# Performance work log

Measured on AMD Instinct MI355X. Metric: run time of the kernel, lower is better.

The kernel has to match this reference:

```python
import jax, jax.numpy as jnp
from jax import lax
import numpy as np

D_IN = 12      # latent_dim / flow input_dim
HALF = 6       # coupling split
HID = 192      # flow_hidden_dim
LAYERS = 24    # flow_layers
N_BASES = 66
SYM = 12       # symmetry_dim
OUT_DIM = 6    # rows of tangent frame J_p
B = 16384
EPS_P = 1e-3
CLAMP = 2.0    # soft clamp for 'exp_clamp' scale map: s = CLAMP*tanh(raw/CLAMP)


def _mlp(z1, p):
    W1, b1, W2, b2, W3, b3 = p
    h = jax.nn.relu(z1 @ W1.T + b1)
    h = jax.nn.relu(h @ W2.T + b2)
    return h @ W3.T + b3


def _coupling_fwd(z, p):
    # AffineCouplingBlock (split->affine->merge) followed by Permute(swap)
    z1, z2 = z[..., :HALF], z[..., HALF:]
    prm = _mlp(z1, p)
    shift, sraw = prm[..., 0::2], prm[..., 1::2]
    s = CLAMP * jnp.tanh(sraw / CLAMP)
    z2 = z2 * jnp.exp(s) + shift
    # merge [z1, z2'] then swap halves -> [z2', z1]
    return jnp.concatenate([z2, z1], axis=-1), jnp.sum(s, axis=-1)


def _coupling_inv(z, p):
    # inverse of Permute(swap) is swap again
    z = jnp.concatenate([z[..., HALF:], z[..., :HALF]], axis=-1)
    z1, z2 = z[..., :HALF], z[..., HALF:]
    prm = _mlp(z1, p)
    shift, sraw = prm[..., 0::2], prm[..., 1::2]
    s = CLAMP * jnp.tanh(sraw / CLAMP)
    z2 = (z2 - shift) * jnp.exp(-s)
    return jnp.concatenate([z1, z2], axis=-1), -jnp.sum(s, axis=-1)


def flow_forward(z, params):
    def step(c, p):
        z, ld = c
        z, d = _coupling_fwd(z, p)
        return (z, ld + d), None
    (z, ld), _ = lax.scan(step, (z, jnp.zeros(z.shape[:-1], z.dtype)), params)
    return z, ld


def flow_inverse(y, params):
    def step(c, p):
        z, ld = c
        z, d = _coupling_inv(z, p)
        return (z, ld + d), None
    (z, ld), _ = lax.scan(step, (y, jnp.zeros(y.shape[:-1], y.dtype)), params, reverse=True)
    return z, ld


def pullback_tangent(z, v, params):
    # J[b] = v[b] @ d(flow_forward)/dz at z[b], via per-sample vjp
    def one(zb, vb):
        _, vjp_fn = jax.vjp(lambda zz: flow_forward(zz, params)[0], zb)
        return jax.vmap(lambda r: vjp_fn(r)[0])(vb)
    return jax.vmap(one)(z, v)


def kl_divergence(J_p, J_q, log_var_diag):
    b, out_dim, in_dim = J_p.shape
    J_p = J_p / jnp.sqrt(jnp.sum(J_p * J_p))  # global normalization
    S_p = jnp.einsum('bni,bmi->bnm', J_p, J_p)
    S_q = jnp.einsum('bin,bim->bnm', J_q, J_q)
    S_pq = jnp.einsum('bni,bmi->bnm', J_p[:, :, :SYM], J_q)
    D = jnp.exp(-log_var_diag)  # (in_dim,)
    I_p = jnp.eye(out_dim, dtype=J_p.dtype)
    I_q = jnp.eye(SYM, dtype=J_q.dtype)
    M = S_p + EPS_P * I_p
    H = S_q + D[:SYM] * I_q
    norm_M = jnp.maximum(jnp.mean(jnp.diagonal(M, axis1=-2, axis2=-1), -1), 1e-6)
    norm_H = jnp.maximum(jnp.mean(jnp.diagonal(H, axis1=-2, axis2=-1), -1), 1e-6)
    M = M + 1e-3 * norm_M[:, None, None] * I_p
    H = H + 1e-3 * norm_H[:, None, None] * I_q
    Db = D + 1e-3 * norm_H[:, None]  # (b, in_dim)
    trace_p = jnp.einsum('bij,bij,bj->b', J_p, J_p, Db)
    trace_q = jnp.einsum('bij,bij->b', J_q, J_q)
    trace_pq = jnp.einsum('bij,bij->b', S_pq, S_pq)
    trace = (EPS_P + 1e-3 * norm_M) * (jnp.sum(Db, -1) + trace_q) + trace_p + trace_pq
    L_M = jnp.linalg.cholesky(M)
    L_H = jnp.linalg.cholesky(H)
    logdet_M = 2.0 * jnp.sum(jnp.log(jnp.diagonal(L_M, axis1=-2, axis2=-1)), -1)
    logdet_H = 2.0 * jnp.sum(jnp.log(jnp.diagonal(L_H, axis1=-2, axis2=-1)), -1)
    logdet_p = logdet_M + (in_dim - out_dim) * np.float32(np.log(EPS_P))
    logdet_q = logdet_H + jnp.sum(jnp.log(Db[:, SYM:]), -1)
    logdet = -(logdet_p + logdet_q)
    return 0.5 * (trace + logdet - in_dim)


def setup_inputs() -> dict:
    key = jax.random.key(0)
    ks = jax.random.split(key, 10)
    y = jax.random.normal(ks[0], (B, D_IN), jnp.float32)
    J_p = jax.random.normal(ks[1], (B, OUT_DIM, D_IN), jnp.float32)
    sc = 0.05
    W1 = sc * jax.random.normal(ks[2], (LAYERS, HID, HALF), jnp.float32)
    b1 = sc * jax.random.normal(ks[3], (LAYERS, HID), jnp.float32)
    W2 = sc * jax.random.normal(ks[4], (LAYERS, HID, HID), jnp.float32)
    b2 = sc * jax.random.normal(ks[5], (LAYERS, HID), jnp.float32)
    W3 = sc * jax.random.normal(ks[6], (LAYERS, D_IN, HID), jnp.float32)
    b3 = sc * jax.random.normal(ks[7], (LAYERS, D_IN), jnp.float32)
    Wsym = (1.0 / np.sqrt(SYM)) * jax.random.normal(ks[8], (N_BASES, SYM, SYM), jnp.float32)
    log_var_diag = jnp.zeros((D_IN,), jnp.float32)
    return {"y": y, "J_p": J_p, "W1": W1, "b1": b1, "W2": W2, "b2": b2,
            "W3": W3, "b3": b3, "Wsym": Wsym, "log_var_diag": log_var_diag}


def reference(y, J_p, W1, b1, W2, b2, W3, b3, Wsym, log_var_diag):
    params = (W1, b1, W2, b2, W3, b3)
    z, ld = flow_inverse(y, params)
    # DiagGaussian(trainable=False) base log prob = standard normal
    log_prob = ld - 0.5 * D_IN * np.float32(np.log(2.0 * np.pi)) - 0.5 * jnp.sum(z * z, -1)
    Jp = pullback_tangent(z, J_p, params)
    A = Wsym - jnp.swapaxes(Wsym, -1, -2)
    J_q = jnp.einsum('bi,mji->bmj', z[:, :SYM], A)
    kl = kl_divergence(Jp, J_q, log_var_diag)
    return (log_prob, kl)
```

## Files before the change

kernel.cpp:

```cpp
#include <hip/hip_runtime.h>
#include <hip/hip_bf16.h>
#include <math.h>

#define BTOT   16384
#define NLAYER 24
#define HID    192
#define NDIN   12
#define NBASE  66
#define EPSP   1e-3f
#define EPB    32

#define EST 200
#define W3ST 17
#define OB_H1  0
#define OB_G   12800
#define OB_R   89600
#define OB_W1  98816
#define OB_W3F 101888
#define OB_PRM 114944
#define OB_GZ  118016
#define OB_Z1  122624
#define OB_LD  123392
#define OB_ZQ  123520
#define OB_RED 123648
#define SMEM_BYTES 123680

typedef __attribute__((ext_vector_type(8))) short s8v;
typedef __attribute__((ext_vector_type(4))) float f4v;
#define MFMA16(a,b,c) __builtin_amdgcn_mfma_f32_16x16x32_bf16(a,b,c,0,0,0)

__device__ __forceinline__ unsigned short f2bf(float f) {
  unsigned u = __builtin_bit_cast(unsigned, f);
  u += 0x7fffu + ((u >> 16) & 1u);
  return (unsigned short)(u >> 16);
}
__device__ __forceinline__ float bf2f(unsigned short h) {
  unsigned u = ((unsigned)h) << 16;
  return __builtin_bit_cast(float, u);
}
__device__ __forceinline__ unsigned pk2(float a, float b) {
  return (unsigned)f2bf(a) | ((unsigned)f2bf(b) << 16);
}
__device__ __forceinline__ float blo(unsigned u) { return bf2f((unsigned short)(u & 0xffff)); }
__device__ __forceinline__ float bhi(unsigned u) { return bf2f((unsigned short)(u >> 16)); }

__global__ void prep_kernel(const float* __restrict__ W2,
                            unsigned short* __restrict__ w2b,
                            unsigned short* __restrict__ w2t) {
  int idx = blockIdx.x * 256 + threadIdx.x;
  int l   = idx / (HID * HID);
  int rem = idx - l * HID * HID;
  int k   = rem / HID;
  int j   = rem - k * HID;
  w2b[idx] = f2bf(W2[idx]);
  w2t[idx] = f2bf(W2[l * HID * HID + j * HID + k]);
}

__global__ __launch_bounds__(768) void flow_kernel(
    float* __restrict__ yz, float* __restrict__ jp,
    const float* __restrict__ W1, const float* __restrict__ b1,
    const float* __restrict__ b2,
    const float* __restrict__ W3, const float* __restrict__ b3,
    const unsigned short* __restrict__ w2b,
    const unsigned short* __restrict__ w2t,
    float* __restrict__ ws_sum, float* __restrict__ out_lp) {
  extern __shared__ char smraw[];
  unsigned short* sH1b = (unsigned short*)(smraw + OB_H1);
  unsigned short* sGb  = (unsigned short*)(smraw + OB_G);
  float* sW3f = (float*)(smraw + OB_W3F);
  float* sR   = (float*)(smraw + OB_R);
  float* sPRM = (float*)(smraw + OB_PRM);
  float* sGZ  = (float*)(smraw + OB_GZ);
  float* sZ1  = (float*)(smraw + OB_Z1);
  float* sLD  = (float*)(smraw + OB_LD);
  float* sZQ  = (float*)(smraw + OB_ZQ);
  float* sRed = (float*)(smraw + OB_RED);

  const int tid  = threadIdx.x;
  const int lane = tid & 63;
  const int w    = __builtin_amdgcn_readfirstlane(tid >> 6);
  const int e    = tid & 31;
  const int grp  = tid >> 5;
  const int lm   = lane & 15, lq = lane >> 4;
  const int blk  = blockIdx.x;

  float z_a = 0.f, z_b = 0.f;
  if (tid < 192) {
    int i = grp;
    z_a = yz[(blk * EPB + e) * 12 + i];
    z_b = yz[(blk * EPB + e) * 12 + 6 + i];
    sZ1[i * EPB + e] = z_b;
  }
  if (tid < 32) { sLD[tid] = 0.f; sZQ[tid] = 0.f; }
  if (tid == 0) sRed[0] = 0.f;
  for (int idx = tid; idx < 1152; idx += 768) sGZ[idx] = 0.f;
  if (tid < 768) sPRM[tid] = 0.f;
  for (int idx = tid; idx < 72 * EPB; idx += 768) {
    int rt = idx >> 5, ee = idx & 31;
    sR[idx] = jp[(blk * EPB + ee) * 72 + rt];
  }
  __syncthreads();

  for (int l = NLAYER - 1; l >= 0; --l) {
    const float* W1l = W1 + l * HID * 6;
    const float* b1l = b1 + l * HID;
    const float* b2l = b2 + l * HID;
    const float* W3l = W3 + l * NDIN * HID;
    const float* b3l = b3 + l * NDIN;
    const unsigned short* w2bl = w2b + l * HID * HID;
    const unsigned short* w2tl = w2t + l * HID * HID;
    float* cur = sPRM + (l & 1) * 384;
    float* prv = sPRM + ((l + 1) & 1) * 384;

    if (tid < 192) {
      const float* wr = W1l + tid * 6;
      uint4 pk;
      pk.x = pk2(wr[0], wr[1]); pk.y = pk2(wr[2], wr[3]);
      pk.z = pk2(wr[4], wr[5]); pk.w = 0;
      *(uint4*)(smraw + OB_W1 + tid * 16) = pk;
    }
    for (int idx = tid; idx < 2304; idx += 768) {
      int t = idx / 192, j = idx - t * 192;
      sW3f[j * W3ST + t] = W3l[idx];
    }
    if (tid < 384) cur[tid] = 0.f;
    if (l != NLAYER - 1) {
      for (int idx = tid; idx < 1152; idx += 768) {
        int i = idx / 192, rem = idx - i * 192;
        int r = rem >> 5, e5 = rem & 31;
        float r1  = sR[(r * 12 + i) * EPB + e5];
        float r2o = sR[(r * 12 + 6 + i) * EPB + e5];
        float es  = prv[(2 * i + 1) * EPB + e5];
        sR[(r * 12 + i) * EPB + e5]     = r2o + sGZ[i * 192 + rem];
        sR[(r * 12 + 6 + i) * EPB + e5] = r1 * es;
        sGZ[i * 192 + rem] = 0.f;
      }
    }
    {
      float z1v[6];
      #pragma unroll
      for (int i = 0; i < 6; ++i) z1v[i] = sZ1[i * EPB + e];
      int jb8 = grp * 8;
      #pragma unroll
      for (int jj = 0; jj < 8; ++jj) {
        int j = jb8 + jj;
        float acc = b1l[j];
        #pragma unroll
        for (int i = 0; i < 6; ++i) acc = fmaf(W1l[j * 6 + i], z1v[i], acc);
        sH1b[e * EST + j] = f2bf(fmaxf(acc, 0.f));
      }
    }
    __syncthreads();

    {
      f4v acc2[2] = {{0,0,0,0},{0,0,0,0}};
      #pragma unroll 2
      for (int kk = 0; kk < 6; ++kk) {
        int jo = kk * 32 + lq * 8;
        s8v A  = *(const s8v*)(w2bl + (w * 16 + lm) * HID + jo);
        s8v B0 = *(const s8v*)&sH1b[lm * EST + jo];
        s8v B1 = *(const s8v*)&sH1b[(16 + lm) * EST + jo];
        acc2[0] = MFMA16(A, B0, acc2[0]);
        acc2[1] = MFMA16(A, B1, acc2[1]);
      }
      int jb2 = w * 16 + lq * 4;
      float pp[2][12];
      #pragma unroll
      for (int nt = 0; nt < 2; ++nt)
        #pragma unroll
        for (int t = 0; t < 12; ++t) pp[nt][t] = 0.f;
      #pragma unroll
      for (int nt = 0; nt < 2; ++nt) {
        int e2 = nt * 16 + lm;
        float hv[4];
        #pragma unroll
        for (int rg = 0; rg < 4; ++rg)
          hv[rg] = fmaxf(acc2[nt][rg] + b2l[jb2 + rg], 0.f);
        unsigned* dst = (unsigned*)sGb + ((e2 * EST + jb2) >> 1);
        dst[0] = pk2(hv[0], hv[1]);
        dst[1] = pk2(hv[2], hv[3]);
        #pragma unroll
        for (int rg = 0; rg < 4; ++rg) {
          const float* w3r = sW3f + (jb2 + rg) * W3ST;
          float v = hv[rg];
          #pragma unroll
          for (int t = 0; t < 12; ++t) pp[nt][t] = fmaf(w3r[t], v, pp[nt][t]);
        }
      }
      #pragma unroll
      for (int nt = 0; nt < 2; ++nt)
        #pragma unroll
        for (int t = 0; t < 12; ++t) {
          float v = pp[nt][t];
          v += __shfl_xor(v, 16);
          v += __shfl_xor(v, 32);
          if (lane < 16) atomicAdd(&cur[t * EPB + nt * 16 + lane], v);
        }
    }
    __syncthreads();

    if (tid < 192) {
      int i = grp;
      float sh = b3l[2 * i]     + cur[(2 * i) * EPB + e];
      float sr = b3l[2 * i + 1] + cur[(2 * i + 1) * EPB + e];
      float s  = 2.f * tanhf(0.5f * sr);
      float es = expf(s), en = expf(-s);
      float tv = z_a - sh;
      z_a = z_b;
      z_b = tv * en;
      sZ1[i * EPB + e] = z_b;
      cur[(2 * i) * EPB + e]     = tv * (1.f - 0.25f * s * s);
      cur[(2 * i + 1) * EPB + e] = es;
      atomicAdd(&sLD[e], -s);
    }
    __syncthreads();

    {
      float tf[6];
      #pragma unroll
      for (int i = 0; i < 6; ++i) tf[i] = cur[(2 * i) * EPB + e];
      int slab = grp * 8;
      const unsigned* hp = (const unsigned*)&sGb[e * EST + slab];
      unsigned h2d[4];
      #pragma unroll
      for (int c = 0; c < 4; ++c) h2d[c] = hp[c];
      float weff[8][6];
      #pragma unroll
      for (int jj = 0; jj < 8; ++jj) {
        const float* wrow = sW3f + (slab + jj) * W3ST;
        #pragma unroll
        for (int c = 0; c < 6; ++c)
          weff[jj][c] = fmaf(tf[c], wrow[2 * c + 1], wrow[2 * c]);
      }
      #pragma unroll
      for (int r = 0; r < 6; ++r) {
        float g[8];
        #pragma unroll
        for (int jj = 0; jj < 8; ++jj) g[jj] = 0.f;
        #pragma unroll
        for (int c = 0; c < 6; ++c) {
          float r1 = sR[(r * 12 + c) * EPB + e];
          #pragma unroll
          for (int jj = 0; jj < 8; ++jj)
            g[jj] = fmaf(weff[jj][c], r1, g[jj]);
        }
        unsigned* dst = (unsigned*)sGb + (((r * EPB + e) * EST + slab) >> 1);
        #pragma unroll
        for (int pr = 0; pr < 4; ++pr) {
          float v0 = (h2d[pr] & 0xffffu) ? g[2 * pr] : 0.f;
          float v1 = (h2d[pr] >> 16)     ? g[2 * pr + 1] : 0.f;
          dst[pr] = pk2(v0, v1);
        }
      }
    }
    __syncthreads();

    {
      const int mtg3 = (w & 3) * 3;
      const int ntg4 = (w >> 2) * 4;
      f4v acc[3][4] = {{{0,0,0,0},{0,0,0,0},{0,0,0,0},{0,0,0,0}},
                       {{0,0,0,0},{0,0,0,0},{0,0,0,0},{0,0,0,0}},
                       {{0,0,0,0},{0,0,0,0},{0,0,0,0},{0,0,0,0}}};
      #pragma unroll 2
      for (int kk = 0; kk < 6; ++kk) {
        int jo = kk * 32 + lq * 8;
        s8v A[3], B[4];
        #pragma unroll
        for (int p = 0; p < 3; ++p)
          A[p] = *(const s8v*)(w2tl + ((mtg3 + p) * 16 + lm) * HID + jo);
        #pragma unroll
        for (int q = 0; q < 4; ++q)
          B[q] = *(const s8v*)&sGb[((ntg4 + q) * 16 + lm) * EST + jo];
        #pragma unroll
        for (int p = 0; p < 3; ++p)
          #pragma unroll
          for (int q = 0; q < 4; ++q)
            acc[p][q] = MFMA16(A[p], B[q], acc[p][q]);
      }
      float pz[4][6];
      #pragma unroll
      for (int q = 0; q < 4; ++q)
        #pragma unroll
        for (int i = 0; i < 6; ++i) pz[q][i] = 0.f;
      #pragma unroll
      for (int p = 0; p < 3; ++p) {
        int kb = (mtg3 + p) * 16 + lq * 4;
        float w1v[4][6];
        #pragma unroll
        for (int rg = 0; rg < 4; ++rg) {
          uint4 wr = *(const uint4*)(smraw + OB_W1 + (kb + rg) * 16);
          w1v[rg][0] = blo(wr.x); w1v[rg][1] = bhi(wr.x);
          w1v[rg][2] = blo(wr.y); w1v[rg][3] = bhi(wr.y);
          w1v[rg][4] = blo(wr.z); w1v[rg][5] = bhi(wr.z);
        }
        #pragma unroll
        for (int q = 0; q < 4; ++q) {
          int e31 = (((ntg4 + q) & 1) << 4) + lm;
          const unsigned* mp = (const unsigned*)&sH1b[e31 * EST + kb];
          unsigned mm0 = mp[0], mm1 = mp[1];
          unsigned short hb[4] = {
            (unsigned short)(mm0 & 0xffff), (unsigned short)(mm0 >> 16),
            (unsigned short)(mm1 & 0xffff), (unsigned short)(mm1 >> 16)};
          #pragma unroll
          for (int rg = 0; rg < 4; ++rg) {
            float val = hb[rg] ? acc[p][q][rg] : 0.f;
            #pragma unroll
            for (int i = 0; i < 6; ++i)
              pz[q][i] = fmaf(w1v[rg][i], val, pz[q][i]);
          }
        }
      }
      #pragma unroll
      for (int q = 0; q < 4; ++q)
        #pragma unroll
        for (int i = 0; i < 6; ++i) {
          float v = pz[q][i];
          v += __shfl_xor(v, 16);
          v += __shfl_xor(v, 32);
          if (lane < 16) atomicAdd(&sGZ[i * 192 + (ntg4 + q) * 16 + lane], v);
        }
    }
    __syncthreads();
  }

  {
    float* prv0 = sPRM;
    for (int idx = tid; idx < 1152; idx += 768) {
      int i = idx / 192, rem = idx - i * 192;
      int r = rem >> 5, e5 = rem & 31;
      float r1  = sR[(r * 12 + i) * EPB + e5];
      float r2o = sR[(r * 12 + 6 + i) * EPB + e5];
      float es  = prv0[(2 * i + 1) * EPB + e5];
      sR[(r * 12 + i) * EPB + e5]     = r2o + sGZ[i * 192 + rem];
      sR[(r * 12 + 6 + i) * EPB + e5] = r1 * es;
    }
  }
  if (tid < 192) {
    int i = grp;
    yz[(blk * EPB + e) * 12 + i]     = z_a;
    yz[(blk * EPB + e) * 12 + 6 + i] = z_b;
    atomicAdd(&sZQ[e], fmaf(z_a, z_a, z_b * z_b));
  }
  __syncthreads();
  if (tid < 32)
    out_lp[blk * EPB + tid] = sLD[tid] - 11.027262398456072f - 0.5f * sZQ[tid];

  float part = 0.f;
  for (int idx = tid; idx < 72 * EPB; idx += 768) {
    int rt = idx >> 5, ee = idx & 31;
    float v = sR[idx];
    jp[(blk * EPB + ee) * 72 + rt] = v;
    part = fmaf(v, v, part);
  }
  #pragma unroll
  for (int off = 32; off > 0; off >>= 1) part += __shfl_down(part, off, 64);
  if ((tid & 63) == 0) atomicAdd(&sRed[0], part);
  __syncthreads();
  if (tid == 0) atomicAdd(ws_sum, sRed[0]);
}

__global__ __launch_bounds__(256) void kl_kernel(
    const float* __restrict__ zin, const float* __restrict__ jpin,
    const float* __restrict__ Wsym, const float* __restrict__ lvd,
    const float* __restrict__ ws_sum, float* __restrict__ out_kl) {
  int elem = blockIdx.x * 256 + threadIdx.x;
  float z[12];
  #pragma unroll
  for (int i = 0; i < 12; ++i) z[i] = zin[elem * 12 + i];
  float scale = 1.0f / sqrtf(ws_sum[0]);
  float Jp[6][12];
  #pragma unroll
  for (int n = 0; n < 6; ++n)
    #pragma unroll
    for (int j = 0; j < 12; ++j)
      Jp[n][j] = jpin[elem * 72 + n * 12 + j] * scale;

  float Sq[78];
  #pragma unroll
  for (int i = 0; i < 78; ++i) Sq[i] = 0.f;
  float tq = 0.f, tpq = 0.f;

  for (int m = 0; m < NBASE; ++m) {
    const float* Wm = Wsym + m * 144;
    float jq[12];
    #pragma unroll
    for (int j = 0; j < 12; ++j) {
      float acc = 0.f;
      #pragma unroll
      for (int i = 0; i < 12; ++i)
        acc = fmaf(Wm[j * 12 + i] - Wm[i * 12 + j], z[i], acc);
      jq[j] = acc;
    }
    #pragma unroll
    for (int i = 0; i < 12; ++i) {
      tq = fmaf(jq[i], jq[i], tq);
      #pragma unroll
      for (int j = 0; j <= i; ++j)
        Sq[i * (i + 1) / 2 + j] = fmaf(jq[i], jq[j], Sq[i * (i + 1) / 2 + j]);
    }
    #pragma unroll
    for (int n = 0; n < 6; ++n) {
      float d = 0.f;
      #pragma unroll
      for (int j = 0; j < 12; ++j) d = fmaf(Jp[n][j], jq[j], d);
      tpq = fmaf(d, d, tpq);
    }
  }

  float Dv[12], Db[12];
  #pragma unroll
  for (int j = 0; j < 12; ++j) Dv[j] = expf(-lvd[j]);

  float mh = 0.f;
  #pragma unroll
  for (int i = 0; i < 12; ++i) mh += Sq[i * (i + 1) / 2 + i] + Dv[i];
  float norm_H = fmaxf(mh * (1.f / 12.f), 1e-6f);
  #pragma unroll
  for (int i = 0; i < 12; ++i) Sq[i * (i + 1) / 2 + i] += Dv[i] + 1e-3f * norm_H;
  float sumDb = 0.f;
  #pragma unroll
  for (int j = 0; j < 12; ++j) { Db[j] = Dv[j] + 1e-3f * norm_H; sumDb += Db[j]; }

  float M[21];
  #pragma unroll
  for (int n = 0; n < 6; ++n)
    #pragma unroll
    for (int mm = 0; mm <= n; ++mm) {
      float acc = 0.f;
      #pragma unroll
      for (int j = 0; j < 12; ++j) acc = fmaf(Jp[n][j], Jp[mm][j], acc);
      M[n * (n + 1) / 2 + mm] = acc;
    }
  float md = 0.f;
  #pragma unroll
  for (int i = 0; i < 6; ++i) md += M[i * (i + 1) / 2 + i];
  float norm_M = fmaxf(md * (1.f / 6.f) + EPSP, 1e-6f);
  #pragma unroll
  for (int i = 0; i < 6; ++i) M[i * (i + 1) / 2 + i] += EPSP + 1e-3f * norm_M;

  float trace_p = 0.f;
  #pragma unroll
  for (int n = 0; n < 6; ++n)
    #pragma unroll
    for (int j = 0; j < 12; ++j)
      trace_p = fmaf(Jp[n][j] * Jp[n][j], Db[j], trace_p);

  float trace = (EPSP + 1e-3f * norm_M) * (sumDb + tq) + trace_p + tpq;

  float ldM = 0.f;
  #pragma unroll
  for (int jc = 0; jc < 6; ++jc) {
    float d = M[jc * (jc + 1) / 2 + jc];
    #pragma unroll
    for (int k = 0; k < jc; ++k) d -= M[jc * (jc + 1) / 2 + k] * M[jc * (jc + 1) / 2 + k];
    d = sqrtf(d);
    ldM += logf(d);
    float di = 1.f / d;
    M[jc * (jc + 1) / 2 + jc] = d;
    #pragma unroll
    for (int i2 = jc + 1; i2 < 6; ++i2) {
      float v = M[i2 * (i2 + 1) / 2 + jc];
      #pragma unroll
      for (int k = 0; k < jc; ++k) v -= M[i2 * (i2 + 1) / 2 + k] * M[jc * (jc + 1) / 2 + k];
      M[i2 * (i2 + 1) / 2 + jc] = v * di;
    }
  }

  float ldH = 0.f;
  #pragma unroll
  for (int jc = 0; jc < 12; ++jc) {
    float d = Sq[jc * (jc + 1) / 2 + jc];
    #pragma unroll
    for (int k = 0; k < jc; ++k) d -= Sq[jc * (jc + 1) / 2 + k] * Sq[jc * (jc + 1) / 2 + k];
    d = sqrtf(d);
    ldH += logf(d);
    float di = 1.f / d;
    Sq[jc * (jc + 1) / 2 + jc] = d;
    #pragma unroll
    for (int i2 = jc + 1; i2 < 12; ++i2) {
      float v = Sq[i2 * (i2 + 1) / 2 + jc];
      #pragma unroll
      for (int k = 0; k < jc; ++k) v -= Sq[i2 * (i2 + 1) / 2 + k] * Sq[jc * (jc + 1) / 2 + k];
      Sq[i2 * (i2 + 1) / 2 + jc] = v * di;
    }
  }

  float logdet_p = 2.f * ldM + 6.f * logf(EPSP);
  float logdet_q = 2.f * ldH;
  out_kl[elem] = 0.5f * (trace - (logdet_p + logdet_q) - 12.f);
}

extern "C" void kernel_launch(void* const* d_in, const int* in_sizes, int n_in,
                              void* d_out, int out_size, void* d_ws, size_t ws_size,
                              hipStream_t stream) {
  (void)in_sizes; (void)n_in; (void)out_size; (void)ws_size;
  float* y    = (float*)d_in[0];
  float* Jp   = (float*)d_in[1];
  const float* W1   = (const float*)d_in[2];
  const float* b1   = (const float*)d_in[3];
  const float* W2   = (const float*)d_in[4];
  const float* b2   = (const float*)d_in[5];
  const float* W3   = (const float*)d_in[6];
  const float* b3   = (const float*)d_in[7];
  const float* Wsym = (const float*)d_in[8];
  const float* lvd  = (const float*)d_in[9];
  float* out = (float*)d_out;

  float* ws_sum = (float*)d_ws;
  unsigned short* w2b = (unsigned short*)((char*)d_ws + 256);
  unsigned short* w2t = (unsigned short*)((char*)d_ws + 256 +
                                          NLAYER * HID * HID * 2);
  hipMemsetAsync(d_ws, 0, 4, stream);

  hipFuncSetAttribute((const void*)flow_kernel,
                      hipFuncAttributeMaxDynamicSharedMemorySize, SMEM_BYTES);

  prep_kernel<<<3456, 256, 0, stream>>>(W2, w2b, w2t);
  flow_kernel<<<BTOT / EPB, 768, SMEM_BYTES, stream>>>(
      y, Jp, W1, b1, b2, W3, b3, w2b, w2t, ws_sum, out);
  kl_kernel<<<64, 256, 0, stream>>>(y, Jp, Wsym, lvd, ws_sum, out + BTOT);
}
```

Baseline: 1.839 ms.

## Split backward tangent GEMM into two halves to shrink LDS and registers

Measured after the change: 3.662 ms. +99.1%, slower.

```diff
diff --git a/kernel.cpp b/kernel.cpp
--- a/kernel.cpp
+++ b/kernel.cpp
@@ -11,19 +11,19 @@
 #define EPB    32
 
 #define EST 200
-#define W3ST 17
+#define W3ST 12
 #define OB_H1  0
 #define OB_G   12800
-#define OB_R   89600
-#define OB_W1  98816
-#define OB_W3F 101888
-#define OB_PRM 114944
-#define OB_GZ  118016
-#define OB_Z1  122624
-#define OB_LD  123392
-#define OB_ZQ  123520
-#define OB_RED 123648
-#define SMEM_BYTES 123680
+#define OB_R   51200
+#define OB_W1  60416
+#define OB_W3F 63488
+#define OB_PRM 72704
+#define OB_GZ  75776
+#define OB_Z1  80384
+#define OB_LD  81152
+#define OB_ZQ  81280
+#define OB_RED 81408
+#define SMEM_BYTES 81440
 
 typedef __attribute__((ext_vector_type(8))) short s8v;
 typedef __attribute__((ext_vector_type(4))) float f4v;
@@ -56,7 +56,7 @@
   w2t[idx] = f2bf(W2[l * HID * HID + j * HID + k]);
 }
 
-__global__ __launch_bounds__(768) void flow_kernel(
+__global__ __launch_bounds__(768, 6) void flow_kernel(
     float* __restrict__ yz, float* __restrict__ jp,
     const float* __restrict__ W1, const float* __restrict__ b1,
     const float* __restrict__ b2,
@@ -215,112 +215,119 @@
     }
     __syncthreads();
 
+    unsigned h2d[4];
     {
-      float tf[6];
-      #pragma unroll
-      for (int i = 0; i < 6; ++i) tf[i] = cur[(2 * i) * EPB + e];
-      int slab = grp * 8;
-      const unsigned* hp = (const unsigned*)&sGb[e * EST + slab];
-      unsigned h2d[4];
+      const unsigned* hp = (const unsigned*)&sGb[e * EST + grp * 8];
       #pragma unroll
       for (int c = 0; c < 4; ++c) h2d[c] = hp[c];
-      float weff[8][6];
-      #pragma unroll
-      for (int jj = 0; jj < 8; ++jj) {
-        const float* wrow = sW3f + (slab + jj) * W3ST;
-        #pragma unroll
-        for (int c = 0; c < 6; ++c)
-          weff[jj][c] = fmaf(tf[c], wrow[2 * c + 1], wrow[2 * c]);
-      }
-      #pragma unroll
-      for (int r = 0; r < 6; ++r) {
-        float g[8];
-        #pragma unroll
-        for (int jj = 0; jj < 8; ++jj) g[jj] = 0.f;
-        #pragma unroll
-        for (int c = 0; c < 6; ++c) {
-          float r1 = sR[(r * 12 + c) * EPB + e];
-          #pragma unroll
-          for (int jj = 0; jj < 8; ++jj)
-            g[jj] = fmaf(weff[jj][c], r1, g[jj]);
+    }
+    #pragma unroll 1
+    for (int hf = 0; hf < 2; ++hf) {
+      {
+        float tf[6];
+        #pragma unroll
+        for (int i = 0; i < 6; ++i) tf[i] = cur[(2 * i) * EPB + e];
+        int slab = grp * 8;
+        float weff[8][6];
+        #pragma unroll
+        for (int jj = 0; jj < 8; ++jj) {
+          const float* wrow = sW3f + (slab + jj) * W3ST;
+          #pragma unroll
+          for (int c = 0; c < 6; ++c)
+            weff[jj][c] = fmaf(tf[c], wrow[2 * c + 1], wrow[2 * c]);
         }
-        unsigned* dst = (unsigned*)sGb + (((r * EPB + e) * EST + slab) >> 1);
-        #pragma unroll
-        for (int pr = 0; pr < 4; ++pr) {
-          float v0 = (h2d[pr] & 0xffffu) ? g[2 * pr] : 0.f;
-          float v1 = (h2d[pr] >> 16)     ? g[2 * pr + 1] : 0.f;
-          dst[pr] = pk2(v0, v1);
-        }
-      }
-    }
-    __syncthreads();
-
-    {
-      const int mtg3 = (w & 3) * 3;
-      const int ntg4 = (w >> 2) * 4;
-      f4v acc[3][4] = {{{0,0,0,0},{0,0,0,0},{0,0,0,0},{0,0,0,0}},
-                       {{0,0,0,0},{0,0,0,0},{0,0,0,0},{0,0,0,0}},
-                       {{0,0,0,0},{0,0,0,0},{0,0,0,0},{0,0,0,0}}};
-      #pragma unroll 2
-      for (int kk = 0; kk < 6; ++kk) {
-        int jo = kk * 32 + lq * 8;
-        s8v A[3], B[4];
-        #pragma unroll
-        for (int p = 0; p < 3; ++p)
-          A[p] = *(const s8v*)(w2tl + ((mtg3 + p) * 16 + lm) * HID + jo);
-        #pragma unroll
-        for (int q = 0; q < 4; ++q)
-          B[q] = *(const s8v*)&sGb[((ntg4 + q) * 16 + lm) * EST + jo];
-        #pragma unroll
-        for (int p = 0; p < 3; ++p)
-          #pragma unroll
-          for (int q = 0; q < 4; ++q)
-            acc[p][q] = MFMA16(A[p], B[q], acc[p][q]);
-      }
-      float pz[4][6];
-      #pragma unroll
-      for (int q = 0; q < 4; ++q)
-        #pragma unroll
-        for (int i = 0; i < 6; ++i) pz[q][i] = 0.f;
-      #pragma unroll
-      for (int p = 0; p < 3; ++p) {
-        int kb = (mtg3 + p) * 16 + lq * 4;
-        float w1v[4][6];
-        #pragma unroll
-        for (int rg = 0; rg < 4; ++rg) {
-          uint4 wr = *(const uint4*)(smraw + OB_W1 + (kb + rg) * 16);
-          w1v[rg][0] = blo(wr.x); w1v[rg][1] = bhi(wr.x);
-          w1v[rg][2] = blo(wr.y); w1v[rg][3] = bhi(wr.y);
-          w1v[rg][4] = blo(wr.z); w1v[rg][5] = bhi(wr.z);
-        }
-        #pragma unroll
-        for (int q = 0; q < 4; ++q) {
-          int e31 = (((ntg4 + q) & 1) << 4) + lm;
-          const unsigned* mp = (const unsigned*)&sH1b[e31 * EST + kb];
-          unsigned mm0 = mp[0], mm1 = mp[1];
-          unsigned short hb[4] = {
-            (unsigned short)(mm0 & 0xffff), (unsigned short)(mm0 >> 16),
-            (unsigned short)(mm1 & 0xffff), (unsigned short)(mm1 >> 16)};
-          #pragma unroll
-          for (int rg = 0; rg < 4; ++rg) {
-            float val = hb[rg] ? acc[p][q][rg] : 0.f;
+        #pragma unroll
+        for (int r = 0; r < 3; ++r) {
+          float g[8];
+          #pragma unroll
+          for (int jj = 0; jj < 8; ++jj) g[jj] = 0.f;
+          #pragma unroll
+          for (int c = 0; c < 6; ++c) {
+            float r1 = sR[((3 * hf + r) * 12 + c) * EPB + e];
             #pragma unroll
-            for (int i = 0; i < 6; ++i)
-              pz[q][i] = fmaf(w1v[rg][i], val, pz[q][i]);
+            for (int jj = 0; jj < 8; ++jj)
+              g[jj] = fmaf(weff[jj][c], r1, g[jj]);
+          }
+          unsigned* dst = (unsigned*)sGb + (((r * EPB + e) * EST + slab) >> 1);
+          #pragma unroll
+          for (int pr = 0; pr < 4; ++pr) {
+            float v0 = (h2d[pr] & 0xffffu) ? g[2 * pr] : 0.f;
+            float v1 = (h2d[pr] >> 16)     ? g[2 * pr + 1] : 0.f;
+            dst[pr] = pk2(v0, v1);
           }
         }
       }
-      #pragma unroll
-      for (int q = 0; q < 4; ++q)
-        #pragma unroll
-        for (int i = 0; i < 6; ++i) {
-          float v = pz[q][i];
-          v += __shfl_xor(v, 16);
-          v += __shfl_xor(v, 32);
-          if (lane < 16) atomicAdd(&sGZ[i * 192 + (ntg4 + q) * 16 + lane], v);
+      __syncthreads();
+
+      {
+        const int mtg3 = (w & 3) * 3;
+        const int ntg2 = (w >> 2) * 2;
+        f4v acc[3][2] = {{{0,0,0,0},{0,0,0,0}},
+                         {{0,0,0,0},{0,0,0,0}},
+                         {{0,0,0,0},{0,0,0,0}}};
+        #pragma unroll 2
+        for (int kk = 0; kk < 6; ++kk) {
+          int jo = kk * 32 + lq * 8;
+          s8v A[3], Bv[2];
+          #pragma unroll
+          for (int p = 0; p < 3; ++p)
+            A[p] = *(const s8v*)(w2tl + ((mtg3 + p) * 16 + lm) * HID + jo);
+          #pragma unroll
+          for (int q = 0; q < 2; ++q)
+            Bv[q] = *(const s8v*)&sGb[((ntg2 + q) * 16 + lm) * EST + jo];
+          #pragma unroll
+          for (int p = 0; p < 3; ++p)
+            #pragma unroll
+            for (int q = 0; q < 2; ++q)
+              acc[p][q] = MFMA16(A[p], Bv[q], acc[p][q]);
         }
-    }
-    __syncthreads();
+        float pz[2][6];
+        #pragma unroll
+        for (int q = 0; q < 2; ++q)
+          #pragma unroll
+          for (int i = 0; i < 6; ++i) pz[q][i] = 0.f;
+        #pragma unroll
+        for (int p = 0; p < 3; ++p) {
+          int kb = (mtg3 + p) * 16 + lq * 4;
+          float w1v[4][6];
+          #pragma unroll
+          for (int rg = 0; rg < 4; ++rg) {
+            uint4 wr = *(const uint4*)(smraw + OB_W1 + (kb + rg) * 16);
+            w1v[rg][0] = blo(wr.x); w1v[rg][1] = bhi(wr.x);
+            w1v[rg][2] = blo(wr.y); w1v[rg][3] = bhi(wr.y);
+            w1v[rg][4] = blo(wr.z); w1v[rg][5] = bhi(wr.z);
+          }
+          #pragma unroll
+          for (int q = 0; q < 2; ++q) {
+            int ntG = hf * 6 + ntg2 + q;
+            int e31 = ((ntG & 1) << 4) + lm;
+            const unsigned* mp = (const unsigned*)&sH1b[e31 * EST + kb];
+            unsigned mm0 = mp[0], mm1 = mp[1];
+            unsigned short hb[4] = {
+              (unsigned short)(mm0 & 0xffff), (unsigned short)(mm0 >> 16),
+              (unsigned short)(mm1 & 0xffff), (unsigned short)(mm1 >> 16)};
+            #pragma unroll
+            for (int rg = 0; rg < 4; ++rg) {
+              float val = hb[rg] ? acc[p][q][rg] : 0.f;
+              #pragma unroll
+              for (int i = 0; i < 6; ++i)
+                pz[q][i] = fmaf(w1v[rg][i], val, pz[q][i]);
+            }
+          }
+        }
+        #pragma unroll
+        for (int q = 0; q < 2; ++q)
+          #pragma unroll
+          for (int i = 0; i < 6; ++i) {
+            float v = pz[q][i];
+            v += __shfl_xor(v, 16);
+            v += __shfl_xor(v, 32);
+            if (lane < 16)
+              atomicAdd(&sGZ[i * 192 + (hf * 6 + ntg2 + q) * 16 + lane], v);
+          }
+      }
+      __syncthreads();
+    }
   }
 
   {
```

## Double elements per block to 64 and split backward GEMM into two halves

Applied to the files above, without the earlier changes.

Measured after the change: 1.747 ms. -5.0%, faster.

```diff
diff --git a/kernel.cpp b/kernel.cpp
--- a/kernel.cpp
+++ b/kernel.cpp
@@ -8,22 +8,22 @@
 #define NDIN   12
 #define NBASE  66
 #define EPSP   1e-3f
-#define EPB    32
+#define EPB    64
 
 #define EST 200
-#define W3ST 17
+#define W3ST 12
 #define OB_H1  0
-#define OB_G   12800
-#define OB_R   89600
-#define OB_W1  98816
-#define OB_W3F 101888
-#define OB_PRM 114944
-#define OB_GZ  118016
-#define OB_Z1  122624
-#define OB_LD  123392
-#define OB_ZQ  123520
-#define OB_RED 123648
-#define SMEM_BYTES 123680
+#define OB_G   25600
+#define OB_R   102400
+#define OB_W1  120832
+#define OB_W3F 123904
+#define OB_PRM 133120
+#define OB_GZ  139264
+#define OB_Z1  148480
+#define OB_LD  150016
+#define OB_ZQ  150272
+#define OB_RED 150528
+#define SMEM_BYTES 150560
 
 typedef __attribute__((ext_vector_type(8))) short s8v;
 typedef __attribute__((ext_vector_type(4))) float f4v;
@@ -79,24 +79,21 @@
   const int tid  = threadIdx.x;
   const int lane = tid & 63;
   const int w    = __builtin_amdgcn_readfirstlane(tid >> 6);
-  const int e    = tid & 31;
-  const int grp  = tid >> 5;
   const int lm   = lane & 15, lq = lane >> 4;
   const int blk  = blockIdx.x;
 
   float z_a = 0.f, z_b = 0.f;
-  if (tid < 192) {
-    int i = grp;
-    z_a = yz[(blk * EPB + e) * 12 + i];
-    z_b = yz[(blk * EPB + e) * 12 + 6 + i];
-    sZ1[i * EPB + e] = z_b;
-  }
-  if (tid < 32) { sLD[tid] = 0.f; sZQ[tid] = 0.f; }
+  if (tid < 384) {
+    z_a = yz[(blk * EPB + lane) * 12 + w];
+    z_b = yz[(blk * EPB + lane) * 12 + 6 + w];
+    sZ1[w * EPB + lane] = z_b;
+  }
+  if (tid < 64) { sLD[tid] = 0.f; sZQ[tid] = 0.f; }
   if (tid == 0) sRed[0] = 0.f;
-  for (int idx = tid; idx < 1152; idx += 768) sGZ[idx] = 0.f;
-  if (tid < 768) sPRM[tid] = 0.f;
+  for (int idx = tid; idx < 2304; idx += 768) sGZ[idx] = 0.f;
+  for (int idx = tid; idx < 1536; idx += 768) sPRM[idx] = 0.f;
   for (int idx = tid; idx < 72 * EPB; idx += 768) {
-    int rt = idx >> 5, ee = idx & 31;
+    int rt = idx >> 6, ee = idx & 63;
     sR[idx] = jp[(blk * EPB + ee) * 72 + rt];
   }
   __syncthreads();
@@ -109,8 +106,8 @@
     const float* b3l = b3 + l * NDIN;
     const unsigned short* w2bl = w2b + l * HID * HID;
     const unsigned short* w2tl = w2t + l * HID * HID;
-    float* cur = sPRM + (l & 1) * 384;
-    float* prv = sPRM + ((l + 1) & 1) * 384;
+    float* cur = sPRM + (l & 1) * 768;
+    float* prv = sPRM + ((l + 1) & 1) * 768;
 
     if (tid < 192) {
       const float* wr = W1l + tid * 6;
@@ -123,54 +120,58 @@
       int t = idx / 192, j = idx - t * 192;
       sW3f[j * W3ST + t] = W3l[idx];
     }
-    if (tid < 384) cur[tid] = 0.f;
+    cur[tid] = 0.f;
     if (l != NLAYER - 1) {
-      for (int idx = tid; idx < 1152; idx += 768) {
-        int i = idx / 192, rem = idx - i * 192;
-        int r = rem >> 5, e5 = rem & 31;
+      for (int idx = tid; idx < 2304; idx += 768) {
+        int i = idx / 384, rem = idx - i * 384;
+        int r = rem >> 6, e5 = rem & 63;
         float r1  = sR[(r * 12 + i) * EPB + e5];
         float r2o = sR[(r * 12 + 6 + i) * EPB + e5];
         float es  = prv[(2 * i + 1) * EPB + e5];
-        sR[(r * 12 + i) * EPB + e5]     = r2o + sGZ[i * 192 + rem];
+        sR[(r * 12 + i) * EPB + e5]     = r2o + sGZ[i * 384 + rem];
         sR[(r * 12 + 6 + i) * EPB + e5] = r1 * es;
-        sGZ[i * 192 + rem] = 0.f;
+        sGZ[i * 384 + rem] = 0.f;
       }
     }
     {
       float z1v[6];
       #pragma unroll
-      for (int i = 0; i < 6; ++i) z1v[i] = sZ1[i * EPB + e];
-      int jb8 = grp * 8;
-      #pragma unroll
-      for (int jj = 0; jj < 8; ++jj) {
-        int j = jb8 + jj;
+      for (int i = 0; i < 6; ++i) z1v[i] = sZ1[i * EPB + lane];
+      int jb = w * 16;
+      float hv[16];
+      #pragma unroll
+      for (int jj = 0; jj < 16; ++jj) {
+        int j = jb + jj;
         float acc = b1l[j];
         #pragma unroll
         for (int i = 0; i < 6; ++i) acc = fmaf(W1l[j * 6 + i], z1v[i], acc);
-        sH1b[e * EST + j] = f2bf(fmaxf(acc, 0.f));
+        hv[jj] = fmaxf(acc, 0.f);
       }
+      uint4 o0, o1;
+      o0.x = pk2(hv[0], hv[1]);  o0.y = pk2(hv[2], hv[3]);
+      o0.z = pk2(hv[4], hv[5]);  o0.w = pk2(hv[6], hv[7]);
+      o1.x = pk2(hv[8], hv[9]);  o1.y = pk2(hv[10], hv[11]);
+      o1.z = pk2(hv[12], hv[13]); o1.w = pk2(hv[14], hv[15]);
+      *(uint4*)&sH1b[lane * EST + jb]     = o0;
+      *(uint4*)&sH1b[lane * EST + jb + 8] = o1;
     }
     __syncthreads();
 
     {
-      f4v acc2[2] = {{0,0,0,0},{0,0,0,0}};
+      f4v acc2[4] = {{0,0,0,0},{0,0,0,0},{0,0,0,0},{0,0,0,0}};
       #pragma unroll 2
       for (int kk = 0; kk < 6; ++kk) {
         int jo = kk * 32 + lq * 8;
-        s8v A  = *(const s8v*)(w2bl + (w * 16 + lm) * HID + jo);
-        s8v B0 = *(const s8v*)&sH1b[lm * EST + jo];
-        s8v B1 = *(const s8v*)&sH1b[(16 + lm) * EST + jo];
-        acc2[0] = MFMA16(A, B0, acc2[0]);
-        acc2[1] = MFMA16(A, B1, acc2[1]);
+        s8v A = *(const s8v*)(w2bl + (w * 16 + lm) * HID + jo);
+        #pragma unroll
+        for (int nt = 0; nt < 4; ++nt) {
+          s8v Bv = *(const s8v*)&sH1b[(nt * 16 + lm) * EST + jo];
+          acc2[nt] = MFMA16(A, Bv, acc2[nt]);
+        }
       }
       int jb2 = w * 16 + lq * 4;
-      float pp[2][12];
-      #pragma unroll
-      for (int nt = 0; nt < 2; ++nt)
-        #pragma unroll
-        for (int t = 0; t < 12; ++t) pp[nt][t] = 0.f;
-      #pragma unroll
-      for (int nt = 0; nt < 2; ++nt) {
+      #pragma unroll
+      for (int nt = 0; nt < 4; ++nt) {
         int e2 = nt * 16 + lm;
         float hv[4];
         #pragma unroll
@@ -179,175 +180,191 @@
         unsigned* dst = (unsigned*)sGb + ((e2 * EST + jb2) >> 1);
         dst[0] = pk2(hv[0], hv[1]);
         dst[1] = pk2(hv[2], hv[3]);
+        float pp[12];
+        #pragma unroll
+        for (int t = 0; t < 12; ++t) pp[t] = 0.f;
         #pragma unroll
         for (int rg = 0; rg < 4; ++rg) {
           const float* w3r = sW3f + (jb2 + rg) * W3ST;
           float v = hv[rg];
           #pragma unroll
-          for (int t = 0; t < 12; ++t) pp[nt][t] = fmaf(w3r[t], v, pp[nt][t]);
+          for (int t = 0; t < 12; ++t) pp[t] = fmaf(w3r[t], v, pp[t]);
         }
-      }
-      #pragma unroll
-      for (int nt = 0; nt < 2; ++nt)
         #pragma unroll
         for (int t = 0; t < 12; ++t) {
-          float v = pp[nt][t];
+          float v = pp[t];
           v += __shfl_xor(v, 16);
           v += __shfl_xor(v, 32);
           if (lane < 16) atomicAdd(&cur[t * EPB + nt * 16 + lane], v);
         }
+      }
     }
     __syncthreads();
 
-    if (tid < 192) {
-      int i = grp;
-      float sh = b3l[2 * i]     + cur[(2 * i) * EPB + e];
-      float sr = b3l[2 * i + 1] + cur[(2 * i + 1) * EPB + e];
+    if (tid < 384) {
+      int i = w;
+      float sh = b3l[2 * i]     + cur[(2 * i) * EPB + lane];
+      float sr = b3l[2 * i + 1] + cur[(2 * i + 1) * EPB + lane];
       float s  = 2.f * tanhf(0.5f * sr);
       float es = expf(s), en = expf(-s);
       float tv = z_a - sh;
       z_a = z_b;
       z_b = tv * en;
-      sZ1[i * EPB + e] = z_b;
-      cur[(2 * i) * EPB + e]     = tv * (1.f - 0.25f * s * s);
-      cur[(2 * i + 1) * EPB + e] = es;
-      atomicAdd(&sLD[e], -s);
+      sZ1[i * EPB + lane] = z_b;
+      cur[(2 * i) * EPB + lane]     = tv * (1.f - 0.25f * s * s);
+      cur[(2 * i + 1) * EPB + lane] = es;
+      atomicAdd(&sLD[lane], -s);
     }
     __syncthreads();
 
+    unsigned h2d[8];
     {
-      float tf[6];
-      #pragma unroll
-      for (int i = 0; i < 6; ++i) tf[i] = cur[(2 * i) * EPB + e];
-      int slab = grp * 8;
-      const unsigned* hp = (const unsigned*)&sGb[e * EST + slab];
-      unsigned h2d[4];
-      #pragma unroll
-      for (int c = 0; c < 4; ++c) h2d[c] = hp[c];
-      float weff[8][6];
-      #pragma unroll
-      for (int jj = 0; jj < 8; ++jj) {
-        const float* wrow = sW3f + (slab + jj) * W3ST;
-        #pragma unroll
-        for (int c = 0; c < 6; ++c)
-          weff[jj][c] = fmaf(tf[c], wrow[2 * c + 1], wrow[2 * c]);
-      }
-      #pragma unroll
-      for (int r = 0; r < 6; ++r) {
-        float g[8];
-        #pragma unroll
-        for (int jj = 0; jj < 8; ++jj) g[jj] = 0.f;
-        #pragma unroll
-        for (int c = 0; c < 6; ++c) {
-          float r1 = sR[(r * 12 + c) * EPB + e];
-          #pragma unroll
-          for (int jj = 0; jj < 8; ++jj)
-            g[jj] = fmaf(weff[jj][c], r1, g[jj]);
-        }
-        unsigned* dst = (unsigned*)sGb + (((r * EPB + e) * EST + slab) >> 1);
-        #pragma unroll
-        for (int pr = 0; pr < 4; ++pr) {
-          float v0 = (h2d[pr] & 0xffffu) ? g[2 * pr] : 0.f;
-          float v1 = (h2d[pr] >> 16)     ? g[2 * pr + 1] : 0.f;
-          dst[pr] = pk2(v0, v1);
-        }
-      }
-    }
-    __syncthreads();
-
-    {
-      const int mtg3 = (w & 3) * 3;
-      const int ntg4 = (w >> 2) * 4;
-      f4v acc[3][4] = {{{0,0,0,0},{0,0,0,0},{0,0,0,0},{0,0,0,0}},
-                       {{0,0,0,0},{0,0,0,0},{0,0,0,0},{0,0,0,0}},
-                       {{0,0,0,0},{0,0,0,0},{0,0,0,0},{0,0,0,0}}};
-      #pragma unroll 2
-      for (int kk = 0; kk < 6; ++kk) {
-        int jo = kk * 32 + lq * 8;
-        s8v A[3], B[4];
-        #pragma unroll
-        for (int p = 0; p < 3; ++p)
-          A[p] = *(const s8v*)(w2tl + ((mtg3 + p) * 16 + lm) * HID + jo);
-        #pragma unroll
-        for (int q = 0; q < 4; ++q)
-          B[q] = *(const s8v*)&sGb[((ntg4 + q) * 16 + lm) * EST + jo];
-        #pragma unroll
-        for (int p = 0; p < 3; ++p)
-          #pragma unroll
-          for (int q = 0; q < 4; ++q)
-            acc[p][q] = MFMA16(A[p], B[q], acc[p][q]);
-      }
-      float pz[4][6];
-      #pragma unroll
-      for (int q = 0; q < 4; ++q)
-        #pragma unroll
-        for (int i = 0; i < 6; ++i) pz[q][i] = 0.f;
-      #pragma unroll
-      for (int p = 0; p < 3; ++p) {
-        int kb = (mtg3 + p) * 16 + lq * 4;
-        float w1v[4][6];
-        #pragma unroll
-        for (int rg = 0; rg < 4; ++rg) {
-          uint4 wr = *(const uint4*)(smraw + OB_W1 + (kb + rg) * 16);
-          w1v[rg][0] = blo(wr.x); w1v[rg][1] = bhi(wr.x);
-          w1v[rg][2] = blo(wr.y); w1v[rg][3] = bhi(wr.y);
-          w1v[rg][4] = blo(wr.z); w1v[rg][5] = bhi(wr.z);
-        }
-        #pragma unroll
-        for (int q = 0; q < 4; ++q) {
-          int e31 = (((ntg4 + q) & 1) << 4) + lm;
-          const unsigned* mp = (const unsigned*)&sH1b[e31 * EST + kb];
-          unsigned mm0 = mp[0], mm1 = mp[1];
-          unsigned short hb[4] = {
-            (unsigned short)(mm0 & 0xffff), (unsigned short)(mm0 >> 16),
-            (unsigned short)(mm1 & 0xffff), (unsigned short)(mm1 >> 16)};
-          #pragma unroll
-          for (int rg = 0; rg < 4; ++rg) {
-            float val = hb[rg] ? acc[p][q][rg] : 0.f;
+      const unsigned* hp = (const unsigned*)&sGb[lane * EST + w * 16];
+      #pragma unroll
+      for (int c = 0; c < 8; ++c) h2d[c] = hp[c];
+    }
+    #pragma unroll 1
+    for (int hf = 0; hf < 2; ++hf) {
+      {
+        float tf[6];
+        #pragma unroll
+        for (int c = 0; c < 6; ++c) tf[c] = cur[(2 * c) * EPB + lane];
+        float r1[3][6];
+        #pragma unroll
+        for (int r = 0; r < 3; ++r)
+          #pragma unroll
+          for (int c = 0; c < 6; ++c)
+            r1[r][c] = sR[((3 * hf + r) * 12 + c) * EPB + lane];
+        #pragma unroll
+        for (int g0 = 0; g0 < 2; ++g0) {
+          int j0 = w * 16 + g0 * 8;
+          float weff[8][6];
+          #pragma unroll
+          for (int jj = 0; jj < 8; ++jj) {
+            const float* wrow = sW3f + (j0 + jj) * W3ST;
             #pragma unroll
-            for (int i = 0; i < 6; ++i)
-              pz[q][i] = fmaf(w1v[rg][i], val, pz[q][i]);
+            for (int c = 0; c < 6; ++c)
+              weff[jj][c] = fmaf(tf[c], wrow[2 * c + 1], wrow[2 * c]);
+          }
+          #pragma unroll
+          for (int r = 0; r < 3; ++r) {
+            float g[8];
+            #pragma unroll
+            for (int jj = 0; jj < 8; ++jj) g[jj] = 0.f;
+            #pragma unroll
+            for (int c = 0; c < 6; ++c) {
+              float rv = r1[r][c];
+              #pragma unroll
+              for (int jj = 0; jj < 8; ++jj)
+                g[jj] = fmaf(weff[jj][c], rv, g[jj]);
+            }
+            unsigned m0 = h2d[g0 * 4 + 0], m1 = h2d[g0 * 4 + 1];
+            unsigned m2 = h2d[g0 * 4 + 2], m3 = h2d[g0 * 4 + 3];
+            uint4 ov;
+            ov.x = pk2((m0 & 0xffffu) ? g[0] : 0.f, (m0 >> 16) ? g[1] : 0.f);
+            ov.y = pk2((m1 & 0xffffu) ? g[2] : 0.f, (m1 >> 16) ? g[3] : 0.f);
+            ov.z = pk2((m2 & 0xffffu) ? g[4] : 0.f, (m2 >> 16) ? g[5] : 0.f);
+            ov.w = pk2((m3 & 0xffffu) ? g[6] : 0.f, (m3 >> 16) ? g[7] : 0.f);
+            *(uint4*)&sGb[(r * EPB + lane) * EST + j0] = ov;
           }
         }
       }
-      #pragma unroll
-      for (int q = 0; q < 4; ++q)
-        #pragma unroll
-        for (int i = 0; i < 6; ++i) {
-          float v = pz[q][i];
-          v += __shfl_xor(v, 16);
-          v += __shfl_xor(v, 32);
-          if (lane < 16) atomicAdd(&sGZ[i * 192 + (ntg4 + q) * 16 + lane], v);
+      __syncthreads();
+
+      {
+        const int mtg3 = (w & 3) * 3;
+        const int ntg4 = (w >> 2) * 4;
+        f4v acc[3][4] = {{{0,0,0,0},{0,0,0,0},{0,0,0,0},{0,0,0,0}},
+                         {{0,0,0,0},{0,0,0,0},{0,0,0,0},{0,0,0,0}},
+                         {{0,0,0,0},{0,0,0,0},{0,0,0,0},{0,0,0,0}}};
+        #pragma unroll 2
+        for (int kk = 0; kk < 6; ++kk) {
+          int jo = kk * 32 + lq * 8;
+          s8v A[3], Bv[4];
+          #pragma unroll
+          for (int p = 0; p < 3; ++p)
+            A[p] = *(const s8v*)(w2tl + ((mtg3 + p) * 16 + lm) * HID + jo);
+          #pragma unroll
+          for (int q = 0; q < 4; ++q)
+            Bv[q] = *(const s8v*)&sGb[((ntg4 + q) * 16 + lm) * EST + jo];
+          #pragma unroll
+          for (int p = 0; p < 3; ++p)
+            #pragma unroll
+            for (int q = 0; q < 4; ++q)
+              acc[p][q] = MFMA16(A[p], Bv[q], acc[p][q]);
         }
-    }
-    __syncthreads();
+        float pz[4][6];
+        #pragma unroll
+        for (int q = 0; q < 4; ++q)
+          #pragma unroll
+          for (int i = 0; i < 6; ++i) pz[q][i] = 0.f;
+        #pragma unroll
+        for (int p = 0; p < 3; ++p) {
+          int kb = (mtg3 + p) * 16 + lq * 4;
+          float w1v[4][6];
+          #pragma unroll
+          for (int rg = 0; rg < 4; ++rg) {
+            uint4 wr = *(const uint4*)(smraw + OB_W1 + (kb + rg) * 16);
+            w1v[rg][0] = blo(wr.x); w1v[rg][1] = bhi(wr.x);
+            w1v[rg][2] = blo(wr.y); w1v[rg][3] = bhi(wr.y);
+            w1v[rg][4] = blo(wr.z); w1v[rg][5] = bhi(wr.z);
+          }
+          #pragma unroll
+          for (int q = 0; q < 4; ++q) {
+            int e63 = (((ntg4 + q) & 3) << 4) + lm;
+            const unsigned* mp = (const unsigned*)&sH1b[e63 * EST + kb];
+            unsigned mm0 = mp[0], mm1 = mp[1];
+            unsigned short hb[4] = {
+              (unsigned short)(mm0 & 0xffff), (unsigned short)(mm0 >> 16),
+              (unsigned short)(mm1 & 0xffff), (unsigned short)(mm1 >> 16)};
+            #pragma unroll
+            for (int rg = 0; rg < 4; ++rg) {
+              float val = hb[rg] ? acc[p][q][rg] : 0.f;
+              #pragma unroll
+              for (int i = 0; i < 6; ++i)
+                pz[q][i] = fmaf(w1v[rg][i], val, pz[q][i]);
+            }
+          }
+        }
+        #pragma unroll
+        for (int q = 0; q < 4; ++q)
+          #pragma unroll
+          for (int i = 0; i < 6; ++i) {
+            float v = pz[q][i];
+            v += __shfl_xor(v, 16);
+            v += __shfl_xor(v, 32);
+            if (lane < 16)
+              atomicAdd(&sGZ[i * 384 + hf * 192 + (ntg4 + q) * 16 + lane], v);
+          }
+      }
+      __syncthreads();
+    }
   }
 
   {
     float* prv0 = sPRM;
-    for (int idx = tid; idx < 1152; idx += 768) {
-      int i = idx / 192, rem = idx - i * 192;
-      int r = rem >> 5, e5 = rem & 31;
+    for (int idx = tid; idx < 2304; idx += 768) {
+      int i = idx / 384, rem = idx - i * 384;
+      int r = rem >> 6, e5 = rem & 63;
       float r1  = sR[(r * 12 + i) * EPB + e5];
       float r2o = sR[(r * 12 + 6 + i) * EPB + e5];
       float es  = prv0[(2 * i + 1) * EPB + e5];
-      sR[(r * 12 + i) * EPB + e5]     = r2o + sGZ[i * 192 + rem];
+      sR[(r * 12 + i) * EPB + e5]     = r2o + sGZ[i * 384 + rem];
       sR[(r * 12 + 6 + i) * EPB + e5] = r1 * es;
     }
   }
-  if (tid < 192) {
-    int i = grp;
-    yz[(blk * EPB + e) * 12 + i]     = z_a;
-    yz[(blk * EPB + e) * 12 + 6 + i] = z_b;
-    atomicAdd(&sZQ[e], fmaf(z_a, z_a, z_b * z_b));
+  if (tid < 384) {
+    yz[(blk * EPB + lane) * 12 + w]     = z_a;
+    yz[(blk * EPB + lane) * 12 + 6 + w] = z_b;
+    atomicAdd(&sZQ[lane], fmaf(z_a, z_a, z_b * z_b));
   }
   __syncthreads();
-  if (tid < 32)
+  if (tid < 64)
     out_lp[blk * EPB + tid] = sLD[tid] - 11.027262398456072f - 0.5f * sZQ[tid];
 
   float part = 0.f;
   for (int idx = tid; idx < 72 * EPB; idx += 768) {
-    int rt = idx >> 5, ee = idx & 31;
+    int rt = idx >> 6, ee = idx & 63;
     float v = sR[idx];
     jp[(blk * EPB + ee) * 72 + rt] = v;
     part = fmaf(v, v, part);
```
